# Performance work log

Hardware: AMD Instinct MI355X
Metric: run time of the kernel (lower is better)

## Reference

```python
import jax, jax.numpy as jnp
import numpy as np

N_NODES = 50000
N_EDGES = 800000
IN_C, HID_C, OUT_C = 128, 256, 64


def _linear_params(key, fan_in, fan_out):
    kw, kb = jax.random.split(key)
    bound = 1.0 / np.sqrt(fan_in)
    w = jax.random.uniform(kw, (fan_in, fan_out), jnp.float32, -bound, bound)
    b = jax.random.uniform(kb, (fan_out,), jnp.float32, -bound, bound)
    return w, b


def setup_inputs() -> dict:
    key = jax.random.key(0)
    ks = jax.random.split(key, 8)
    x = jax.random.normal(ks[0], (N_NODES, IN_C), jnp.float32)
    edge_index = jax.random.randint(ks[1], (2, N_EDGES), 0, N_NODES, dtype=jnp.int64)
    w1a, b1a = _linear_params(ks[2], IN_C, HID_C)
    w1b, b1b = _linear_params(ks[3], HID_C, HID_C)
    w2a, b2a = _linear_params(ks[4], HID_C, HID_C)
    w2b, b2b = _linear_params(ks[5], HID_C, HID_C)
    w3a, b3a = _linear_params(ks[6], HID_C, HID_C)
    w3b, b3b = _linear_params(ks[7], HID_C, OUT_C)
    return {
        "x": x, "edge_index": edge_index,
        "w1a": w1a, "b1a": b1a, "w1b": w1b, "b1b": b1b,
        "w2a": w2a, "b2a": b2a, "w2b": w2b, "b2b": b2b,
        "w3a": w3a, "b3a": b3a, "w3b": w3b, "b3b": b3b,
    }


def _gin_conv(x, src, dst, wa, ba, wb, bb):
    # GINConv (eps=0): MLP( x + sum_{j->i} x_j )
    agg = jax.ops.segment_sum(x[src], dst, num_segments=N_NODES)  # [N, d]
    h = x + agg
    h = jnp.maximum(h @ wa + ba, 0.0)
    return h @ wb + bb


def reference(x, edge_index, w1a, b1a, w1b, b1b, w2a, b2a, w2b, b2b,
              w3a, b3a, w3b, b3b):
    src, dst = edge_index[0], edge_index[1]
    h = jnp.maximum(_gin_conv(x, src, dst, w1a, b1a, w1b, b1b), 0.0)
    h = jnp.maximum(_gin_conv(h, src, dst, w2a, b2a, w2b, b2b), 0.0)
    # output head: Linear -> ReLU -> Dropout(eval: identity) -> Linear
    h = jnp.maximum(h @ w3a + b3a, 0.0)
    return h @ w3b + b3b  # [N, OUT_C]
```

## Files before the change

kernel.cpp:

```cpp
#include <hip/hip_runtime.h>
#include <stdint.h>

#define N_NODES 50000
#define N_EDGES 800000
#define M_PAD   50048
#define NREP    4
#define MCAP    8
#define SCAP    24
#define BCAP    (MCAP + SCAP)
#define CSTR    50048
#define NPX     6256

typedef __attribute__((ext_vector_type(8))) short bf16x8;
typedef __attribute__((ext_vector_type(4))) float f32x4;
typedef __attribute__((ext_vector_type(4))) unsigned int u32x4;

__device__ __forceinline__ unsigned short f2b(float f){
    unsigned int u = __builtin_bit_cast(unsigned int, f);
    u += 0x7fffu + ((u >> 16) & 1u);
    return (unsigned short)(u >> 16);
}
__device__ __forceinline__ float b2f(unsigned short s){
    unsigned int u = ((unsigned int)s) << 16;
    return __builtin_bit_cast(float, u);
}
__device__ __forceinline__ float bcf(unsigned int u){
    return __builtin_bit_cast(float, u);
}

__device__ __forceinline__ void gl_lds16(const void* g, void* l){
    __builtin_amdgcn_global_load_lds(
        (const __attribute__((address_space(1))) void*)g,
        (__attribute__((address_space(3))) void*)l, 16, 0, 0);
}

__device__ __forceinline__ int t_off(int row, int us){
    return row * 256 + (((us >> 3) ^ (row & 7)) << 3) + (us & 7);
}

__device__ __forceinline__ int pdeg(const int* __restrict__ cnt, int n){
    int v = 0;
#pragma unroll
    for (int r = 0; r < 4; ++r){
        int c = cnt[r * CSTR + n];
        v += (c > BCAP) ? BCAP : c;
    }
    return (v + 3) & ~3;
}

__global__ void k_x2b(const float* __restrict__ x, unsigned short* __restrict__ xs,
                      int* __restrict__ cnt){
    int gi = blockIdx.x * 256 + threadIdx.x;
    if (gi < NREP * CSTR) cnt[gi] = 0;
    size_t e0 = (size_t)gi * 8;
    if (e0 >= (size_t)M_PAD * 128) return;
    int node = (int)(e0 >> 7);
    int ch0  = (int)(e0 & 127);
    int sl = ch0 >> 5, wth = ch0 & 31;
    bf16x8 o;
    if (node < N_NODES){
        const float4* xp = (const float4*)(x + e0);
        float4 a = xp[0], b = xp[1];
        o[0] = (short)f2b(a.x); o[1] = (short)f2b(a.y);
        o[2] = (short)f2b(a.z); o[3] = (short)f2b(a.w);
        o[4] = (short)f2b(b.x); o[5] = (short)f2b(b.y);
        o[6] = (short)f2b(b.z); o[7] = (short)f2b(b.w);
    } else {
#pragma unroll
        for (int i = 0; i < 8; ++i) o[i] = 0;
    }
    *(bf16x8*)&xs[((size_t)(sl * 50048 + node)) * 32 + wth] = o;
}

__global__ __launch_bounds__(256) void k_scatter(const int* __restrict__ ei,
        int* __restrict__ cnt, unsigned short* __restrict__ mn,
        unsigned short* __restrict__ sp){
    const int x = blockIdx.x & 7;
    const int c = blockIdx.x >> 3;
    const int nlo = x * NPX, nhi = nlo + NPX;
    const int r = threadIdx.x & 3;
#pragma unroll
    for (int i = 0; i < 4; ++i){
        int e = c * 1024 + i * 256 + threadIdx.x;
        if (e < N_EDGES){
            int d = ei[N_EDGES + e];
            if (d >= nlo && d < nhi && (unsigned)d < N_NODES){
                unsigned s = (unsigned)ei[e];
                if (s < N_NODES){
                    int p = atomicAdd(&cnt[r * CSTR + d], 1);
                    int b = (d << 2) + r;
                    if (p < MCAP) mn[(b << 3) + p] = (unsigned short)s;
                    else if (p < BCAP) sp[b * SCAP + (p - MCAP)] = (unsigned short)s;
                }
            }
        }
    }
}

__global__ void k_scan1(const int* __restrict__ cnt, int* __restrict__ bsum){
    __shared__ int s[256];
    int t = threadIdx.x, n = blockIdx.x * 256 + t;
    int v = (n < M_PAD) ? pdeg(cnt, n) : 0;
    s[t] = v;
    __syncthreads();
    for (int off = 128; off > 0; off >>= 1){
        if (t < off) s[t] += s[t + off];
        __syncthreads();
    }
    if (t == 0) bsum[blockIdx.x] = s[0];
}

__global__ void k_scan2(const int* __restrict__ bsum, int* __restrict__ boff){
    __shared__ int s[256];
    int t = threadIdx.x;
    int v = (t < 196) ? bsum[t] : 0;
    s[t] = v;
    __syncthreads();
    for (int off = 1; off < 256; off <<= 1){
        int a = (t >= off) ? s[t - off] : 0;
        __syncthreads();
        s[t] += a;
        __syncthreads();
    }
    boff[t] = s[t] - v;
}

__global__ void k_scan3(const int* __restrict__ cnt, const int* __restrict__ boff,
                        int* __restrict__ mgoff){
    __shared__ int s[256];
    int t = threadIdx.x, n = blockIdx.x * 256 + t;
    int v = (n < M_PAD) ? pdeg(cnt, n) : 0;
    s[t] = v;
    __syncthreads();
    for (int off = 1; off < 256; off <<= 1){
        int a = (t >= off) ? s[t - off] : 0;
        __syncthreads();
        s[t] += a;
        __syncthreads();
    }
    if (n < M_PAD) mgoff[n] = boff[blockIdx.x] + s[t] - v;
}

__global__ void k_merge(const int* __restrict__ cnt, const int* __restrict__ mgoff,
                        const unsigned short* __restrict__ mn, const unsigned short* __restrict__ sp,
                        unsigned short* __restrict__ mg, int* __restrict__ mginfo,
                        unsigned short* __restrict__ lperm){
    __shared__ unsigned int keys[64];
    const int t = threadIdx.x;
    const int r = t & 3;
    const int n = blockIdx.x * 64 + (t >> 2);
    int c = cnt[r * CSTR + n];
    if (c > BCAP) c = BCAP;

    const unsigned short* src  = &mn[((n << 2) + r) << 3];
    const unsigned short* ssrc = &sp[((n << 2) + r) * SCAP];
    unsigned short v[BCAP];
    {
        ushort4 m0 = *(const ushort4*)(src);
        ushort4 m1 = *(const ushort4*)(src + 4);
        v[0]=m0.x; v[1]=m0.y; v[2]=m0.z; v[3]=m0.w;
        v[4]=m1.x; v[5]=m1.y; v[6]=m1.z; v[7]=m1.w;
#pragma unroll
        for (int q = 0; q < 6; ++q){
            ushort4 sq = *(const ushort4*)(ssrc + q * 4);
            v[8 + q*4 + 0] = sq.x; v[8 + q*4 + 1] = sq.y;
            v[8 + q*4 + 2] = sq.z; v[8 + q*4 + 3] = sq.w;
        }
    }
#pragma unroll
    for (int i = 0; i < BCAP; ++i)
        if (i >= c) v[i] = 0xFFFFu;

#pragma unroll
    for (int k = 2; k <= 32; k <<= 1){
#pragma unroll
        for (int j = k >> 1; j > 0; j >>= 1){
#pragma unroll
            for (int i = 0; i < 32; ++i){
                const int l = i ^ j;
                if (l > i){
                    const bool up = ((i & k) == 0);
                    unsigned short a = v[i], b = v[l];
                    bool sw = up ? (a > b) : (a < b);
                    unsigned short lo = sw ? b : a, hi = sw ? a : b;
                    v[i] = lo; v[l] = hi;
                }
            }
        }
    }

    int incl = c;
    int t1 = __shfl_up(incl, 1, 4); if (r >= 1) incl += t1;
    int t2 = __shfl_up(incl, 2, 4); if (r >= 2) incl += t2;
    const int excl = incl - c;
    const int total = __shfl(incl, 3, 4);
    const unsigned mb = (unsigned)mgoff[n];
#pragma unroll
    for (int i = 0; i < BCAP; ++i)
        if (i < c) mg[mb + excl + i] = v[i];
    if (r == 3){
        int grp = (total + 3) >> 2;
        mginfo[n] = ((int)mb << 6) | grp;
        for (int pos = total; pos < grp * 4; ++pos) mg[mb + pos] = (unsigned short)N_NODES;
        keys[t >> 2] = ((unsigned)grp << 6) | (unsigned)(t >> 2);
    }
    __syncthreads();
    for (int k = 2; k <= 64; k <<= 1){
        for (int j = k >> 1; j > 0; j >>= 1){
            if (t < 64){
                int l = t ^ j;
                if (l > t){
                    bool up = ((t & k) == 0);
                    unsigned a = keys[t], b = keys[l];
                    if (up ? (a > b) : (a < b)){ keys[t] = b; keys[l] = a; }
                }
            }
            __syncthreads();
        }
    }
    if (t < 64)
        lperm[blockIdx.x * 64 + t] = (unsigned short)(blockIdx.x * 64 + (keys[t] & 63));
}

template<int C, bool SPLIT>
__global__ __launch_bounds__(256) void k_aggx(const unsigned short* __restrict__ in,
        const int* __restrict__ mginfo, const unsigned short* __restrict__ mg,
        const unsigned short* __restrict__ lperm, unsigned short* __restrict__ out){
    constexpr int RS = C / 8;
    const int bid = blockIdx.x, w8 = bid & 7;
    int g, nbase;
    if (SPLIT){ g = w8 & 3; nbase = ((bid >> 3) + (w8 >> 2) * 391) * 64; }
    else      { g = w8;     nbase = (bid >> 3) * 64; }
    const int lane = threadIdx.x & 63, wid = threadIdx.x >> 6;
    const int qd = lane >> 2, lq = lane & 3;
    const int n = (int)lperm[nbase + wid * 16 + qd];
    const u32x4* __restrict__ xr = (const u32x4*)in;
    const unsigned sbu = (unsigned)g * 50048u;

    float alo[4], ahi[4];
    {
        u32x4 s = xr[(sbu + (unsigned)n) * 4u + (unsigned)lq];
#pragma unroll
        for (int j = 0; j < 4; ++j){
            alo[j] = bcf(s[j] << 16);
            ahi[j] = bcf(s[j] & 0xFFFF0000u);
        }
    }
    const int info = mginfo[n];
    const int grp = info & 63;
    const unsigned mbase = (unsigned)(info >> 6);
    for (int k = 0; k < grp; ++k){
        ushort4 jj = *(const ushort4*)&mg[mbase + (unsigned)(k * 4)];
        u32x4 v0 = xr[(sbu + jj.x) * 4u + lq];
        u32x4 v1 = xr[(sbu + jj.y) * 4u + lq];
        u32x4 v2 = xr[(sbu + jj.z) * 4u + lq];
        u32x4 v3 = xr[(sbu + jj.w) * 4u + lq];
#pragma unroll
        for (int j = 0; j < 4; ++j){
            alo[j] += (bcf(v0[j] << 16) + bcf(v1[j] << 16))
                    + (bcf(v2[j] << 16) + bcf(v3[j] << 16));
            ahi[j] += (bcf(v0[j] & 0xFFFF0000u) + bcf(v1[j] & 0xFFFF0000u))
                    + (bcf(v2[j] & 0xFFFF0000u) + bcf(v3[j] & 0xFFFF0000u));
        }
    }
    bf16x8 o;
#pragma unroll
    for (int j = 0; j < 4; ++j){
        o[2*j]     = (short)f2b(alo[j]);
        o[2*j + 1] = (short)f2b(ahi[j]);
    }
    *(bf16x8*)&out[((unsigned)n * RS + (unsigned)(g * 4 + lq)) * 8u] = o;
}

__global__ void k_wt_all(const float* w0, const float* w1, const float* w2,
                         const float* w3, const float* w4, const float* w5,
                         unsigned short* o0, unsigned short* o1, unsigned short* o2,
                         unsigned short* o3, unsigned short* o4, unsigned short* o5){
    const int Ks[6]  = {128, 256, 256, 256, 256, 256};
    const int Ns[6]  = {256, 256, 256, 256, 256,  64};
    const int NPs[6] = {256, 256, 256, 256, 256, 128};
    int s = blockIdx.y;
    const float* w = (s == 0) ? w0 : (s == 1) ? w1 : (s == 2) ? w2
                   : (s == 3) ? w3 : (s == 4) ? w4 : w5;
    unsigned short* o = (s == 0) ? o0 : (s == 1) ? o1 : (s == 2) ? o2
                      : (s == 3) ? o3 : (s == 4) ? o4 : o5;
    int K = Ks[s], N = Ns[s], NP = NPs[s];
    int idx = blockIdx.x * 256 + threadIdx.x;
    if (idx >= NP * K) return;
    int np = idx / K, k = idx - np * K;
    float v = (np < N) ? w[(size_t)k * N + np] : 0.f;
    o[idx] = f2b(v);
}

template<int K1, int NMID, int NOUT, bool RELU_OUT, bool SLICED>
__global__ __launch_bounds__(256) void k_mlp2(const unsigned short* __restrict__ A,
        const unsigned short* __restrict__ WA, const float* __restrict__ bA,
        const unsigned short* __restrict__ WB, const float* __restrict__ bB,
        void* __restrict__ out, int mstore){
    constexpr int NFA = NMID / 32;
    constexpr int NFB = NOUT / 32;
    __shared__ alignas(16) unsigned short As[64 * 32];
    __shared__ alignas(16) unsigned short Bs[NMID * 32];
    __shared__ alignas(16) unsigned short T[64 * 256];
    const int tid  = threadIdx.x;
    const int lane = tid & 63;
    const int c = lane & 15, qq = lane >> 4;
    const int sc = (qq ^ (c & 3)) * 8;
    const int row0 = blockIdx.x * 64;
    const int wm = (tid >> 6) >> 1, wn = (tid >> 6) & 1;

    const f32x4 fzero = {0.f, 0.f, 0.f, 0.f};
    const char* Ab = (const char*)A;

    {
        f32x4 acc[NFA][2];
#pragma unroll
        for (int nf = 0; nf < NFA; ++nf){ acc[nf][0] = fzero; acc[nf][1] = fzero; }
        const char* Wb = (const char*)WA;
        for (int kt = 0; kt < K1 / 32; ++kt){
            {
                const int o = tid * 16;
                const int row = o >> 6, gs = ((o & 63) >> 4) ^ (row & 3);
                gl_lds16(Ab + ((size_t)(row0 + row) * K1 + kt * 32) * 2 + gs * 16,
                         (char*)As + o);
            }
#pragma unroll
            for (int ch = 0; ch < NMID / 64; ++ch){
                const int o = ch * 4096 + tid * 16;
                const int row = o >> 6, gs = ((o & 63) >> 4) ^ (row & 3);
                gl_lds16(Wb + ((size_t)row * K1 + kt * 32) * 2 + gs * 16,
                         (char*)Bs + o);
            }
            __syncthreads();
            bf16x8 xf[2];
#pragma unroll
            for (int mf = 0; mf < 2; ++mf)
                xf[mf] = *(const bf16x8*)&As[(wm * 32 + mf * 16 + c) * 32 + sc];
#pragma unroll
            for (int nf = 0; nf < NFA; ++nf){
                bf16x8 wf = *(const bf16x8*)&Bs[((wn * NFA + nf) * 16 + c) * 32 + sc];
#pragma unroll
                for (int mf = 0; mf < 2; ++mf)
                    acc[nf][mf] = __builtin_amdgcn_mfma_f32_16x16x32_bf16(wf, xf[mf], acc[nf][mf], 0, 0, 0);
            }
            __syncthreads();
        }
#pragma unroll
        for (int nf = 0; nf < NFA; ++nf){
            const int nb = wn * (NFA * 16) + nf * 16 + qq * 4;
            const float4 bb = *(const float4*)&bA[nb];
#pragma unroll
            for (int mf = 0; mf < 2; ++mf){
                const int ml = wm * 32 + mf * 16 + c;
                float v0 = fmaxf(acc[nf][mf][0] + bb.x, 0.f);
                float v1 = fmaxf(acc[nf][mf][1] + bb.y, 0.f);
                float v2 = fmaxf(acc[nf][mf][2] + bb.z, 0.f);
                float v3 = fmaxf(acc[nf][mf][3] + bb.w, 0.f);
                uint2 p;
                p.x = (unsigned)f2b(v0) | ((unsigned)f2b(v1) << 16);
                p.y = (unsigned)f2b(v2) | ((unsigned)f2b(v3) << 16);
                *(uint2*)&T[t_off(ml, nb)] = p;
            }
        }
    }
    __syncthreads();

    {
        f32x4 acc[NFB][2];
#pragma unroll
        for (int nf = 0; nf < NFB; ++nf){ acc[nf][0] = fzero; acc[nf][1] = fzero; }
        const char* Wb = (const char*)WB;
        for (int kt = 0; kt < NMID / 32; ++kt){
#pragma unroll
            for (int ch = 0; ch < NOUT / 64; ++ch){
                const int o = ch * 4096 + tid * 16;
                const int row = o >> 6, gs = ((o & 63) >> 4) ^ (row & 3);
                gl_lds16(Wb + ((size_t)row * NMID + kt * 32) * 2 + gs * 16,
                         (char*)Bs + o);
            }
            __syncthreads();
            bf16x8 xf[2];
#pragma unroll
            for (int mf = 0; mf < 2; ++mf){
                const int rr = wm * 32 + mf * 16 + c;
                xf[mf] = *(const bf16x8*)&T[t_off(rr, kt * 32 + qq * 8)];
            }
#pragma unroll
            for (int nf = 0; nf < NFB; ++nf){
                bf16x8 wf = *(const bf16x8*)&Bs[((wn * NFB + nf) * 16 + c) * 32 + sc];
#pragma unroll
                for (int mf = 0; mf < 2; ++mf)
                    acc[nf][mf] = __builtin_amdgcn_mfma_f32_16x16x32_bf16(wf, xf[mf], acc[nf][mf], 0, 0, 0);
            }
            __syncthreads();
        }
#pragma unroll
        for (int nf = 0; nf < NFB; ++nf){
            const int nb = wn * (NFB * 16) + nf * 16 + qq * 4;
            const float4 bb = *(const float4*)&bB[nb];
#pragma unroll
            for (int mf = 0; mf < 2; ++mf){
                const int m = row0 + wm * 32 + mf * 16 + c;
                if (m < mstore){
                    float v0 = acc[nf][mf][0] + bb.x;
                    float v1 = acc[nf][mf][1] + bb.y;
                    float v2 = acc[nf][mf][2] + bb.z;
                    float v3 = acc[nf][mf][3] + bb.w;
                    if (RELU_OUT){
                        v0 = fmaxf(v0, 0.f); v1 = fmaxf(v1, 0.f);
                        v2 = fmaxf(v2, 0.f); v3 = fmaxf(v3, 0.f);
                    }
                    uint2 p;
                    p.x = (unsigned)f2b(v0) | ((unsigned)f2b(v1) << 16);
                    p.y = (unsigned)f2b(v2) | ((unsigned)f2b(v3) << 16);
                    if (SLICED){
                        if (m >= N_NODES){ p.x = 0; p.y = 0; }
                        *(uint2*)&((unsigned short*)out)[
                            ((size_t)((nb >> 5) * 50048 + m)) * 32 + (nb & 31)] = p;
                    } else {
                        *(uint2*)&((unsigned short*)out)[(size_t)m * NOUT + nb] = p;
                    }
                }
            }
        }
    }
}

__global__ __launch_bounds__(256) void k_mlp4(const unsigned short* __restrict__ A,
        const unsigned short* __restrict__ W1, const float* __restrict__ B1,
        const unsigned short* __restrict__ W2, const float* __restrict__ B2,
        const unsigned short* __restrict__ W3, const float* __restrict__ B3,
        const unsigned short* __restrict__ W4, const float* __restrict__ B4,
        float* __restrict__ out){
    __shared__ alignas(16) unsigned short As[64 * 32];
    __shared__ alignas(16) unsigned short Bs[256 * 32];
    __shared__ alignas(16) unsigned short T[64 * 256];
    const int tid  = threadIdx.x;
    const int lane = tid & 63;
    const int c = lane & 15, qq = lane >> 4;
    const int sc = (qq ^ (c & 3)) * 8;
    const int row0 = blockIdx.x * 64;
    const int wm = (tid >> 6) >> 1, wn = (tid >> 6) & 1;
    const f32x4 fzero = {0.f, 0.f, 0.f, 0.f};

    {
        f32x4 acc[8][2];
#pragma unroll
        for (int nf = 0; nf < 8; ++nf){ acc[nf][0] = fzero; acc[nf][1] = fzero; }
        const char* Ab = (const char*)A;
        const char* Wb = (const char*)W1;
        for (int kt = 0; kt < 8; ++kt){
            {
                const int o = tid * 16;
                const int row = o >> 6, gs = ((o & 63) >> 4) ^ (row & 3);
                gl_lds16(Ab + ((size_t)(row0 + row) * 256 + kt * 32) * 2 + gs * 16,
                         (char*)As + o);
            }
#pragma unroll
            for (int ch = 0; ch < 4; ++ch){
                const int o = ch * 4096 + tid * 16;
                const int row = o >> 6, gs = ((o & 63) >> 4) ^ (row & 3);
                gl_lds16(Wb + ((size_t)row * 256 + kt * 32) * 2 + gs * 16,
                         (char*)Bs + o);
            }
            __syncthreads();
            bf16x8 xf[2];
#pragma unroll
            for (int mf = 0; mf < 2; ++mf)
                xf[mf] = *(const bf16x8*)&As[(wm * 32 + mf * 16 + c) * 32 + sc];
#pragma unroll
            for (int nf = 0; nf < 8; ++nf){
                bf16x8 wf = *(const bf16x8*)&Bs[((wn * 8 + nf) * 16 + c) * 32 + sc];
#pragma unroll
                for (int mf = 0; mf < 2; ++mf)
                    acc[nf][mf] = __builtin_amdgcn_mfma_f32_16x16x32_bf16(wf, xf[mf], acc[nf][mf], 0, 0, 0);
            }
            __syncthreads();
        }
#pragma unroll
        for (int nf = 0; nf < 8; ++nf){
            const int nb = wn * 128 + nf * 16 + qq * 4;
            const float4 bb = *(const float4*)&B1[nb];
#pragma unroll
            for (int mf = 0; mf < 2; ++mf){
                const int ml = wm * 32 + mf * 16 + c;
                float v0 = fmaxf(acc[nf][mf][0] + bb.x, 0.f);
                float v1 = fmaxf(acc[nf][mf][1] + bb.y, 0.f);
                float v2 = fmaxf(acc[nf][mf][2] + bb.z, 0.f);
                float v3 = fmaxf(acc[nf][mf][3] + bb.w, 0.f);
                uint2 p;
                p.x = (unsigned)f2b(v0) | ((unsigned)f2b(v1) << 16);
                p.y = (unsigned)f2b(v2) | ((unsigned)f2b(v3) << 16);
                *(uint2*)&T[t_off(ml, nb)] = p;
            }
        }
    }
    __syncthreads();

#pragma unroll 1
    for (int st = 0; st < 2; ++st){
        const char* Wb = (const char*)(st == 0 ? W2 : W3);
        const float* Bb = (st == 0 ? B2 : B3);
        f32x4 acc[8][2];
#pragma unroll
        for (int nf = 0; nf < 8; ++nf){ acc[nf][0] = fzero; acc[nf][1] = fzero; }
        for (int kt = 0; kt < 8; ++kt){
#pragma unroll
            for (int ch = 0; ch < 4; ++ch){
                const int o = ch * 4096 + tid * 16;
                const int row = o >> 6, gs = ((o & 63) >> 4) ^ (row & 3);
                gl_lds16(Wb + ((size_t)row * 256 + kt * 32) * 2 + gs * 16,
                         (char*)Bs + o);
            }
            __syncthreads();
            bf16x8 xf[2];
#pragma unroll
            for (int mf = 0; mf < 2; ++mf){
                const int rr = wm * 32 + mf * 16 + c;
                xf[mf] = *(const bf16x8*)&T[t_off(rr, kt * 32 + qq * 8)];
            }
#pragma unroll
            for (int nf = 0; nf < 8; ++nf){
                bf16x8 wf = *(const bf16x8*)&Bs[((wn * 8 + nf) * 16 + c) * 32 + sc];
#pragma unroll
                for (int mf = 0; mf < 2; ++mf)
                    acc[nf][mf] = __builtin_amdgcn_mfma_f32_16x16x32_bf16(wf, xf[mf], acc[nf][mf], 0, 0, 0);
            }
            __syncthreads();
        }
#pragma unroll
        for (int nf = 0; nf < 8; ++nf){
            const int nb = wn * 128 + nf * 16 + qq * 4;
            const float4 bb = *(const float4*)&Bb[nb];
#pragma unroll
            for (int mf = 0; mf < 2; ++mf){
                const int ml = wm * 32 + mf * 16 + c;
                float v0 = fmaxf(acc[nf][mf][0] + bb.x, 0.f);
                float v1 = fmaxf(acc[nf][mf][1] + bb.y, 0.f);
                float v2 = fmaxf(acc[nf][mf][2] + bb.z, 0.f);
                float v3 = fmaxf(acc[nf][mf][3] + bb.w, 0.f);
                uint2 p;
                p.x = (unsigned)f2b(v0) | ((unsigned)f2b(v1) << 16);
                p.y = (unsigned)f2b(v2) | ((unsigned)f2b(v3) << 16);
                *(uint2*)&T[t_off(ml, nb)] = p;
            }
        }
        __syncthreads();
    }

    {
        f32x4 acc[2][2];
#pragma unroll
        for (int nf = 0; nf < 2; ++nf){ acc[nf][0] = fzero; acc[nf][1] = fzero; }
        const char* Wb = (const char*)W4;
        for (int kt = 0; kt < 8; ++kt){
            {
                const int o = tid * 16;
                const int row = o >> 6, gs = ((o & 63) >> 4) ^ (row & 3);
                gl_lds16(Wb + ((size_t)row * 256 + kt * 32) * 2 + gs * 16,
                         (char*)Bs + o);
            }
            __syncthreads();
            bf16x8 xf[2];
#pragma unroll
            for (int mf = 0; mf < 2; ++mf){
                const int rr = wm * 32 + mf * 16 + c;
                xf[mf] = *(const bf16x8*)&T[t_off(rr, kt * 32 + qq * 8)];
            }
#pragma unroll
            for (int nf = 0; nf < 2; ++nf){
                bf16x8 wf = *(const bf16x8*)&Bs[((wn * 2 + nf) * 16 + c) * 32 + sc];
#pragma unroll
                for (int mf = 0; mf < 2; ++mf)
                    acc[nf][mf] = __builtin_amdgcn_mfma_f32_16x16x32_bf16(wf, xf[mf], acc[nf][mf], 0, 0, 0);
            }
            __syncthreads();
        }
#pragma unroll
        for (int nf = 0; nf < 2; ++nf){
            const int nb = wn * 32 + nf * 16 + qq * 4;
            const float4 bb = *(const float4*)&B4[nb];
#pragma unroll
            for (int mf = 0; mf < 2; ++mf){
                const int m = row0 + wm * 32 + mf * 16 + c;
                if (m < N_NODES){
                    float4 p = make_float4(acc[nf][mf][0] + bb.x, acc[nf][mf][1] + bb.y,
                                           acc[nf][mf][2] + bb.z, acc[nf][mf][3] + bb.w);
                    *(float4*)&out[(size_t)m * 64 + nb] = p;
                }
            }
        }
    }
}

extern "C" void kernel_launch(void* const* d_in, const int* in_sizes, int n_in,
                              void* d_out, int out_size, void* d_ws, size_t ws_size,
                              hipStream_t stream){
    const float* x   = (const float*)d_in[0];
    const int*   ei  = (const int*)d_in[1];
    const float* w1a = (const float*)d_in[2];
    const float* b1a = (const float*)d_in[3];
    const float* w1b = (const float*)d_in[4];
    const float* b1b = (const float*)d_in[5];
    const float* w2a = (const float*)d_in[6];
    const float* b2a = (const float*)d_in[7];
    const float* w2b = (const float*)d_in[8];
    const float* b2b = (const float*)d_in[9];
    const float* w3a = (const float*)d_in[10];
    const float* b3a = (const float*)d_in[11];
    const float* w3b = (const float*)d_in[12];
    const float* b3b = (const float*)d_in[13];

    char* ws = (char*)d_ws;
    size_t off = 0;
    auto take = [&](size_t bytes) -> char* {
        off = (off + 255) & ~(size_t)255;
        char* p = ws + off;
        off += bytes;
        return p;
    };
    unsigned short* xs1  = (unsigned short*)take((size_t)4 * 50048 * 32 * 2);
    unsigned short* g1   = (unsigned short*)take((size_t)M_PAD * 128 * 2);
    unsigned short* h1s  = (unsigned short*)take((size_t)8 * 50048 * 32 * 2);
    unsigned short* g2   = (unsigned short*)take((size_t)M_PAD * 256 * 2);
    unsigned short* wt1a = (unsigned short*)take(256 * 128 * 2);
    unsigned short* wt1b = (unsigned short*)take(256 * 256 * 2);
    unsigned short* wt2a = (unsigned short*)take(256 * 256 * 2);
    unsigned short* wt2b = (unsigned short*)take(256 * 256 * 2);
    unsigned short* wt3a = (unsigned short*)take(256 * 256 * 2);
    unsigned short* wt3b = (unsigned short*)take(128 * 256 * 2);
    int*            cnt  = (int*)take((size_t)NREP * CSTR * 4);
    unsigned short* mn   = (unsigned short*)take((size_t)M_PAD * 4 * MCAP * 2);
    unsigned short* sp   = (unsigned short*)take((size_t)M_PAD * 4 * SCAP * 2);
    unsigned short* mg   = (unsigned short*)take((size_t)1100000 * 2);
    int*            mgoff  = (int*)take((size_t)M_PAD * 4);
    int*            mginfo = (int*)take((size_t)M_PAD * 4);
    int*            bsum = (int*)take(256 * 4);
    int*            boff = (int*)take(256 * 4);
    unsigned short* lperm = (unsigned short*)take((size_t)M_PAD * 2);

    k_x2b<<<(M_PAD * 128 / 8 + 255) / 256, 256, 0, stream>>>(x, xs1, cnt);
    k_scatter<<<782 * 8, 256, 0, stream>>>(ei, cnt, mn, sp);
    k_scan1<<<196, 256, 0, stream>>>(cnt, bsum);
    k_scan2<<<1,   256, 0, stream>>>(bsum, boff);
    k_scan3<<<196, 256, 0, stream>>>(cnt, boff, mgoff);
    k_merge<<<782, 256, 0, stream>>>(cnt, mgoff, mn, sp, mg, mginfo, lperm);
    k_wt_all<<<dim3(256, 6), 256, 0, stream>>>(w1a, w1b, w2a, w2b, w3a, w3b,
                                               wt1a, wt1b, wt2a, wt2b, wt3a, wt3b);

    k_aggx<128, true ><<<391 * 8, 256, 0, stream>>>(xs1, mginfo, mg, lperm, g1);
    k_mlp2<128, 256, 256, true, true><<<M_PAD / 64, 256, 0, stream>>>(
        g1, wt1a, b1a, wt1b, b1b, h1s, M_PAD);
    k_aggx<256, false><<<782 * 8, 256, 0, stream>>>(h1s, mginfo, mg, lperm, g2);
    k_mlp4<<<M_PAD / 64, 256, 0, stream>>>(
        g2, wt2a, b2a, wt2b, b2b, wt3a, b3a, wt3b, b3b, (float*)d_out);
}
```

Before: 216.1 us.

## Double-buffer LDS staging in fused MLP kernels to overlap loads with MFMA

Turns the A and weight LDS tiles into double buffers and prefetches the next k-slice (including the first slice of the next layer's weights) while MFMAs run on the current one. This removes one barrier per k-step and hides global-to-LDS latency behind compute. The cost is a larger LDS footprint (the weight buffer now holds two 256-row tiles), which can lower occupancy. There is also a subtle dependency on the asynchronous global_load_lds completing before the trailing barrier.

```diff
diff --git a/kernel.cpp b/kernel.cpp
--- a/kernel.cpp
+++ b/kernel.cpp
@@ -36,6 +36,15 @@
 
 __device__ __forceinline__ int t_off(int row, int us){
     return row * 256 + (((us >> 3) ^ (row & 7)) << 3) + (us & 7);
+}
+
+__device__ __forceinline__ void stage_w(const char* __restrict__ Wb, int kt, int K,
+                                        int nch, int tid, char* dst){
+    for (int ch = 0; ch < nch; ++ch){
+        const int o = ch * 4096 + tid * 16;
+        const int row = o >> 6, gs = ((o & 63) >> 4) ^ (row & 3);
+        gl_lds16(Wb + ((size_t)row * K + kt * 32) * 2 + gs * 16, dst + o);
+    }
 }
 
 __device__ __forceinline__ int pdeg(const int* __restrict__ cnt, int n){
@@ -299,8 +308,10 @@
         void* __restrict__ out, int mstore){
     constexpr int NFA = NMID / 32;
     constexpr int NFB = NOUT / 32;
-    __shared__ alignas(16) unsigned short As[64 * 32];
-    __shared__ alignas(16) unsigned short Bs[NMID * 32];
+    constexpr int KTA = K1 / 32;
+    constexpr int KTB = NMID / 32;
+    __shared__ alignas(16) unsigned short As[2][64 * 32];
+    __shared__ alignas(16) unsigned short Bs[2][256 * 32];
     __shared__ alignas(16) unsigned short T[64 * 256];
     const int tid  = threadIdx.x;
     const int lane = tid & 63;
@@ -311,39 +322,45 @@
 
     const f32x4 fzero = {0.f, 0.f, 0.f, 0.f};
     const char* Ab = (const char*)A;
+    int cur = 0;
+
+    {
+        const int o = tid * 16;
+        const int row = o >> 6, gs = ((o & 63) >> 4) ^ (row & 3);
+        gl_lds16(Ab + ((size_t)(row0 + row) * K1) * 2 + gs * 16, (char*)As[0] + o);
+    }
+    stage_w((const char*)WA, 0, K1, NMID / 64, tid, (char*)Bs[0]);
+    __syncthreads();
 
     {
         f32x4 acc[NFA][2];
 #pragma unroll
         for (int nf = 0; nf < NFA; ++nf){ acc[nf][0] = fzero; acc[nf][1] = fzero; }
-        const char* Wb = (const char*)WA;
-        for (int kt = 0; kt < K1 / 32; ++kt){
-            {
+        for (int kt = 0; kt < KTA; ++kt){
+            if (kt < KTA - 1){
                 const int o = tid * 16;
                 const int row = o >> 6, gs = ((o & 63) >> 4) ^ (row & 3);
-                gl_lds16(Ab + ((size_t)(row0 + row) * K1 + kt * 32) * 2 + gs * 16,
-                         (char*)As + o);
-            }
-#pragma unroll
-            for (int ch = 0; ch < NMID / 64; ++ch){
-                const int o = ch * 4096 + tid * 16;
-                const int row = o >> 6, gs = ((o & 63) >> 4) ^ (row & 3);
-                gl_lds16(Wb + ((size_t)row * K1 + kt * 32) * 2 + gs * 16,
-                         (char*)Bs + o);
-            }
-            __syncthreads();
+                gl_lds16(Ab + ((size_t)(row0 + row) * K1 + (kt + 1) * 32) * 2 + gs * 16,
+                         (char*)As[cur ^ 1] + o);
+                stage_w((const char*)WA, kt + 1, K1, NMID / 64, tid, (char*)Bs[cur ^ 1]);
+            } else {
+                stage_w((const char*)WB, 0, NMID, NOUT / 64, tid, (char*)Bs[cur ^ 1]);
+            }
+            const unsigned short* AsC = As[cur];
+            const unsigned short* BsC = Bs[cur];
             bf16x8 xf[2];
 #pragma unroll
             for (int mf = 0; mf < 2; ++mf)
-                xf[mf] = *(const bf16x8*)&As[(wm * 32 + mf * 16 + c) * 32 + sc];
+                xf[mf] = *(const bf16x8*)&AsC[(wm * 32 + mf * 16 + c) * 32 + sc];
 #pragma unroll
             for (int nf = 0; nf < NFA; ++nf){
-                bf16x8 wf = *(const bf16x8*)&Bs[((wn * NFA + nf) * 16 + c) * 32 + sc];
+                bf16x8 wf = *(const bf16x8*)&BsC[((wn * NFA + nf) * 16 + c) * 32 + sc];
 #pragma unroll
                 for (int mf = 0; mf < 2; ++mf)
                     acc[nf][mf] = __builtin_amdgcn_mfma_f32_16x16x32_bf16(wf, xf[mf], acc[nf][mf], 0, 0, 0);
             }
             __syncthreads();
+            cur ^= 1;
         }
 #pragma unroll
         for (int nf = 0; nf < NFA; ++nf){
@@ -369,16 +386,10 @@
         f32x4 acc[NFB][2];
 #pragma unroll
         for (int nf = 0; nf < NFB; ++nf){ acc[nf][0] = fzero; acc[nf][1] = fzero; }
-        const char* Wb = (const char*)WB;
-        for (int kt = 0; kt < NMID / 32; ++kt){
-#pragma unroll
-            for (int ch = 0; ch < NOUT / 64; ++ch){
-                const int o = ch * 4096 + tid * 16;
-                const int row = o >> 6, gs = ((o & 63) >> 4) ^ (row & 3);
-                gl_lds16(Wb + ((size_t)row * NMID + kt * 32) * 2 + gs * 16,
-                         (char*)Bs + o);
-            }
-            __syncthreads();
+        for (int kt = 0; kt < KTB; ++kt){
+            if (kt < KTB - 1)
+                stage_w((const char*)WB, kt + 1, NMID, NOUT / 64, tid, (char*)Bs[cur ^ 1]);
+            const unsigned short* BsC = Bs[cur];
             bf16x8 xf[2];
 #pragma unroll
             for (int mf = 0; mf < 2; ++mf){
@@ -387,12 +398,13 @@
             }
 #pragma unroll
             for (int nf = 0; nf < NFB; ++nf){
-                bf16x8 wf = *(const bf16x8*)&Bs[((wn * NFB + nf) * 16 + c) * 32 + sc];
+                bf16x8 wf = *(const bf16x8*)&BsC[((wn * NFB + nf) * 16 + c) * 32 + sc];
 #pragma unroll
                 for (int mf = 0; mf < 2; ++mf)
                     acc[nf][mf] = __builtin_amdgcn_mfma_f32_16x16x32_bf16(wf, xf[mf], acc[nf][mf], 0, 0, 0);
             }
             __syncthreads();
+            cur ^= 1;
         }
 #pragma unroll
         for (int nf = 0; nf < NFB; ++nf){
@@ -432,8 +444,8 @@
         const unsigned short* __restrict__ W3, const float* __restrict__ B3,
         const unsigned short* __restrict__ W4, const float* __restrict__ B4,
         float* __restrict__ out){
-    __shared__ alignas(16) unsigned short As[64 * 32];
-    __shared__ alignas(16) unsigned short Bs[256 * 32];
+    __shared__ alignas(16) unsigned short As[2][64 * 32];
+    __shared__ alignas(16) unsigned short Bs[2][256 * 32];
     __shared__ alignas(16) unsigned short T[64 * 256];
     const int tid  = threadIdx.x;
     const int lane = tid & 63;
@@ -442,40 +454,46 @@
     const int row0 = blockIdx.x * 64;
     const int wm = (tid >> 6) >> 1, wn = (tid >> 6) & 1;
     const f32x4 fzero = {0.f, 0.f, 0.f, 0.f};
+    const char* Ab = (const char*)A;
+    int cur = 0;
+
+    {
+        const int o = tid * 16;
+        const int row = o >> 6, gs = ((o & 63) >> 4) ^ (row & 3);
+        gl_lds16(Ab + ((size_t)(row0 + row) * 256) * 2 + gs * 16, (char*)As[0] + o);
+    }
+    stage_w((const char*)W1, 0, 256, 4, tid, (char*)Bs[0]);
+    __syncthreads();
 
     {
         f32x4 acc[8][2];
 #pragma unroll
         for (int nf = 0; nf < 8; ++nf){ acc[nf][0] = fzero; acc[nf][1] = fzero; }
-        const char* Ab = (const char*)A;
-        const char* Wb = (const char*)W1;
         for (int kt = 0; kt < 8; ++kt){
-            {
+            if (kt < 7){
                 const int o = tid * 16;
                 const int row = o >> 6, gs = ((o & 63) >> 4) ^ (row & 3);
-                gl_lds16(Ab + ((size_t)(row0 + row) * 256 + kt * 32) * 2 + gs * 16,
-                         (char*)As + o);
-            }
-#pragma unroll
-            for (int ch = 0; ch < 4; ++ch){
-                const int o = ch * 4096 + tid * 16;
-                const int row = o >> 6, gs = ((o & 63) >> 4) ^ (row & 3);
-                gl_lds16(Wb + ((size_t)row * 256 + kt * 32) * 2 + gs * 16,
-                         (char*)Bs + o);
-            }
-            __syncthreads();
+                gl_lds16(Ab + ((size_t)(row0 + row) * 256 + (kt + 1) * 32) * 2 + gs * 16,
+                         (char*)As[cur ^ 1] + o);
+                stage_w((const char*)W1, kt + 1, 256, 4, tid, (char*)Bs[cur ^ 1]);
+            } else {
+                stage_w((const char*)W2, 0, 256, 4, tid, (char*)Bs[cur ^ 1]);
+            }
+            const unsigned short* AsC = As[cur];
+            const unsigned short* BsC = Bs[cur];
             bf16x8 xf[2];
 #pragma unroll
             for (int mf = 0; mf < 2; ++mf)
-                xf[mf] = *(const bf16x8*)&As[(wm * 32 + mf * 16 + c) * 32 + sc];
+                xf[mf] = *(const bf16x8*)&AsC[(wm * 32 + mf * 16 + c) * 32 + sc];
 #pragma unroll
             for (int nf = 0; nf < 8; ++nf){
-                bf16x8 wf = *(const bf16x8*)&Bs[((wn * 8 + nf) * 16 + c) * 32 + sc];
+                bf16x8 wf = *(const bf16x8*)&BsC[((wn * 8 + nf) * 16 + c) * 32 + sc];
 #pragma unroll
                 for (int mf = 0; mf < 2; ++mf)
                     acc[nf][mf] = __builtin_amdgcn_mfma_f32_16x16x32_bf16(wf, xf[mf], acc[nf][mf], 0, 0, 0);
             }
             __syncthreads();
+            cur ^= 1;
         }
 #pragma unroll
         for (int nf = 0; nf < 8; ++nf){
@@ -499,20 +517,17 @@
 
 #pragma unroll 1
     for (int st = 0; st < 2; ++st){
-        const char* Wb = (const char*)(st == 0 ? W2 : W3);
+        const char* Wb    = (const char*)(st == 0 ? W2 : W3);
+        const char* Wnext = (const char*)(st == 0 ? W3 : W4);
+        const int nchNext = (st == 0) ? 4 : 1;
         const float* Bb = (st == 0 ? B2 : B3);
         f32x4 acc[8][2];
 #pragma unroll
         for (int nf = 0; nf < 8; ++nf){ acc[nf][0] = fzero; acc[nf][1] = fzero; }
         for (int kt = 0; kt < 8; ++kt){
-#pragma unroll
-            for (int ch = 0; ch < 4; ++ch){
-                const int o = ch * 4096 + tid * 16;
-                const int row = o >> 6, gs = ((o & 63) >> 4) ^ (row & 3);
-                gl_lds16(Wb + ((size_t)row * 256 + kt * 32) * 2 + gs * 16,
-                         (char*)Bs + o);
-            }
-            __syncthreads();
+            if (kt < 7) stage_w(Wb, kt + 1, 256, 4, tid, (char*)Bs[cur ^ 1]);
+            else        stage_w(Wnext, 0, 256, nchNext, tid, (char*)Bs[cur ^ 1]);
+            const unsigned short* BsC = Bs[cur];
             bf16x8 xf[2];
 #pragma unroll
             for (int mf = 0; mf < 2; ++mf){
@@ -521,12 +536,13 @@
             }
 #pragma unroll
             for (int nf = 0; nf < 8; ++nf){
-                bf16x8 wf = *(const bf16x8*)&Bs[((wn * 8 + nf) * 16 + c) * 32 + sc];
+                bf16x8 wf = *(const bf16x8*)&BsC[((wn * 8 + nf) * 16 + c) * 32 + sc];
 #pragma unroll
                 for (int mf = 0; mf < 2; ++mf)
                     acc[nf][mf] = __builtin_amdgcn_mfma_f32_16x16x32_bf16(wf, xf[mf], acc[nf][mf], 0, 0, 0);
             }
             __syncthreads();
+            cur ^= 1;
         }
 #pragma unroll
         for (int nf = 0; nf < 8; ++nf){
@@ -552,15 +568,9 @@
         f32x4 acc[2][2];
 #pragma unroll
         for (int nf = 0; nf < 2; ++nf){ acc[nf][0] = fzero; acc[nf][1] = fzero; }
-        const char* Wb = (const char*)W4;
         for (int kt = 0; kt < 8; ++kt){
-            {
-                const int o = tid * 16;
-                const int row = o >> 6, gs = ((o & 63) >> 4) ^ (row & 3);
-                gl_lds16(Wb + ((size_t)row * 256 + kt * 32) * 2 + gs * 16,
-                         (char*)Bs + o);
-            }
-            __syncthreads();
+            if (kt < 7) stage_w((const char*)W4, kt + 1, 256, 1, tid, (char*)Bs[cur ^ 1]);
+            const unsigned short* BsC = Bs[cur];
             bf16x8 xf[2];
 #pragma unroll
             for (int mf = 0; mf < 2; ++mf){
@@ -569,12 +579,13 @@
             }
 #pragma unroll
             for (int nf = 0; nf < 2; ++nf){
-                bf16x8 wf = *(const bf16x8*)&Bs[((wn * 2 + nf) * 16 + c) * 32 + sc];
+                bf16x8 wf = *(const bf16x8*)&BsC[((wn * 2 + nf) * 16 + c) * 32 + sc];
 #pragma unroll
                 for (int mf = 0; mf < 2; ++mf)
                     acc[nf][mf] = __builtin_amdgcn_mfma_f32_16x16x32_bf16(wf, xf[mf], acc[nf][mf], 0, 0, 0);
             }
             __syncthreads();
+            cur ^= 1;
         }
 #pragma unroll
         for (int nf = 0; nf < 2; ++nf){
```

New measurement: 209.6 us. 1.03x faster.
